# Kernel optimization log

Measured on AMD Instinct MI355X. Metric: run time of the kernel, lower is better.

## Reference

```python
import jax, jax.numpy as jnp
import numpy as np

B, T, C, H = 1, 1024, 2048, 32
N = C // H  # head_dim = 64
EPS_GN = 0.00064


def setup_inputs() -> dict:
    key = jax.random.key(0)
    ks = jax.random.split(key, 40)
    f32 = jnp.float32

    def rn(k, shape, s):
        return jax.random.normal(k, shape, f32) * s

    layer_idx, n_layer = 12, 24
    r01 = layer_idx / (n_layer - 1)
    r1a0 = 1.0 - layer_idx / n_layer
    ddd = (jnp.arange(C, dtype=f32) / C).reshape(1, 1, C)
    decay_speed = -7.0 + 5.0 * (jnp.arange(C, dtype=f32) / (C - 1)) ** (0.85 + r01 ** 0.5)

    inp = dict(
        hidden_states=jax.random.normal(ks[0], (B, T, C), f32),
        Wq=rn(ks[1], (C, C), 0.02), Wk=rn(ks[2], (C, C), 0.02),
        Wv=rn(ks[3], (C, C), 0.02), Wo=rn(ks[4], (C, C), 0.02),
        time_maa_x=1.0 - ddd ** (0.6 * r1a0 ** 0.9),
        time_maa_rg=rn(ks[5], (1, 1, C), 0.01),
        time_maa_wa=rn(ks[6], (1, 1, C), 0.01),
        time_maa_k=rn(ks[7], (1, 1, C), 0.01),
        time_maa_v=rn(ks[8], (1, 1, C), 0.01),
        time_maa_w1=rn(ks[9], (C, 4 * 32), 0.01),
        time_maa_w2=rn(ks[10], (4, 32, C), 0.01),
        time_decay=decay_speed.reshape(1, 1, C) + 0.5,
        time_decay_w1=rn(ks[11], (C, 64), 0.01),
        time_decay_w2=rn(ks[12], (64, C), 0.01),
        time_aaaaa=rn(ks[13], (1, 1, C), 0.01),
        time_aaa_w1=rn(ks[14], (C, 16), 0.01),
        time_aaa_w2=rn(ks[15], (16, C), 0.01),
        time_kkk_w1=rn(ks[16], (C, 16), 0.01),
        time_kkk_w2=rn(ks[17], (16, C), 0.01),
        gate_w1=rn(ks[18], (C, 128), 0.01),
        gate_w2=rn(ks[19], (128, C), 0.01),
        time_misc_a=rn(ks[20], (1, 1, C), 0.01),
        ma_w1=rn(ks[21], (C, 16), 0.01),
        ma_w2=rn(ks[22], (16, C), 0.01),
        time_misc_k=rn(ks[23], (1, 1, C), 0.01),
        mk_w1=rn(ks[24], (C, 16), 0.01),
        mk_w2=rn(ks[25], (16, C), 0.01),
        time_faaaa=rn(ks[26], (1, 1, H, N), 0.01),
        ln_w=1.0 + rn(ks[27], (C,), 0.01),
        ln_b=rn(ks[28], (C,), 0.01),
    )
    return inp


def _wkv7(r, w, k, v, a, b):
    """RWKV7 matrix-state recurrence. Inputs [B,T,C]; per head state [N,N].
    state_t = state * exp(w_t) (per key-col) + (state @ a_t) b_t^T + v_t k_t^T;
    out_t = state_t @ r_t."""
    hs = lambda x: x.reshape(B, T, H, N)
    r, k, v, a, b = map(hs, (r, k, v, a, b))
    dec = jnp.exp(hs(w))  # w <= -0.5, decay in (0,1)

    def step(state, inp):
        r_t, d_t, k_t, v_t, a_t, b_t = inp  # each [B,H,N]
        sa = jnp.einsum('bhij,bhj->bhi', state, a_t)
        state = (state * d_t[:, :, None, :]
                 + sa[..., None] * b_t[:, :, None, :]
                 + v_t[..., None] * k_t[:, :, None, :])
        out = jnp.einsum('bhij,bhj->bhi', state, r_t)
        return state, out

    xs = tuple(jnp.moveaxis(t, 1, 0) for t in (r, dec, k, v, a, b))  # [T,B,H,N]
    state0 = jnp.zeros((B, H, N, N), r.dtype)
    _, out = jax.lax.scan(step, state0, xs)
    return jnp.moveaxis(out, 0, 1).reshape(B, T, C)


def _group_norm(x, w, b):
    xg = x.reshape(B, T, H, N)
    mu = xg.mean(-1, keepdims=True)
    var = xg.var(-1, keepdims=True)
    xn = (xg - mu) * jax.lax.rsqrt(var + EPS_GN)
    return xn.reshape(B, T, C) * w + b


def reference(hidden_states, Wq, Wk, Wv, Wo, time_maa_x, time_maa_rg, time_maa_wa,
              time_maa_k, time_maa_v, time_maa_w1, time_maa_w2, time_decay,
              time_decay_w1, time_decay_w2, time_aaaaa, time_aaa_w1, time_aaa_w2,
              time_kkk_w1, time_kkk_w2, gate_w1, gate_w2, time_misc_a, ma_w1, ma_w2,
              time_misc_k, mk_w1, mk_w2, time_faaaa, ln_w, ln_b):
    x = hidden_states  # T already multiple of 16, so no padding branch
    dxprev = jnp.pad(x, ((0, 0), (1, 0), (0, 0)))[:, :-1] - x  # token shift
    xxx = x + dxprev * time_maa_x
    mix = jnp.tanh(xxx @ time_maa_w1).reshape(B, T, 4, 32)
    mix = jnp.einsum('btfd,fdc->fbtc', mix, time_maa_w2)  # [4,B,T,C]
    mrg, mwa, mk_mix, mv = mix[0], mix[1], mix[2], mix[3]
    xrg = x + dxprev * (time_maa_rg + mrg)
    xwa = x + dxprev * (time_maa_wa + mwa)
    xk = x + dxprev * (time_maa_k + mk_mix)
    xv = x + dxprev * (time_maa_v + mv)

    r = xrg @ Wq
    w = -jax.nn.softplus(-(time_decay + jnp.tanh(xwa @ time_decay_w1) @ time_decay_w2)) - 0.5
    k = xk @ Wk
    v = xv @ Wv
    g = jnp.tanh(xrg @ gate_w1) @ gate_w2

    kk = k + jnp.tanh(xk @ time_kkk_w1) @ time_kkk_w2
    kkh = kk.reshape(B, T, H, N)
    kk = (kkh / jnp.maximum(jnp.linalg.norm(kkh, axis=-1, keepdims=True), 1e-12)).reshape(B, T, C)

    a = jax.nn.sigmoid(time_aaaaa + (xwa @ time_aaa_w1) @ time_aaa_w2)
    ma = jax.nn.sigmoid(time_misc_a + (xwa @ ma_w1) @ ma_w2)
    k = k * ma + k * a * (1.0 - ma)
    mk_g = jax.nn.sigmoid(time_misc_k + (xk @ mk_w1) @ mk_w2)
    k = k * jnp.exp(jnp.minimum(w * mk_g, 0.0))

    y = _wkv7(r, w, k, v, -kk, kk * a)
    y = _group_norm(y, ln_w, ln_b)
    rh, kh, vh = (t.reshape(B, T, H, N) for t in (r, k, v))
    y = y + ((rh * kh * time_faaaa).sum(-1, keepdims=True) * vh).reshape(B, T, C)
    return (y * g) @ Wo
```

## Files before the change

### kernel.cpp

```cpp
#include <hip/hip_runtime.h>


#define T_ 1024
#define C_ 2048
#define H_ 32
#define N_ 64

using half8  = __attribute__((ext_vector_type(8))) _Float16;
using half4  = __attribute__((ext_vector_type(4))) _Float16;
using floatx4 = __attribute__((ext_vector_type(4))) float;

#define DPP_ADD(v, ctrl) \
    ((v) + __int_as_float(__builtin_amdgcn_update_dpp( \
        0, __float_as_int(v), (ctrl), 0xf, 0xf, true)))
#define REDUCE16(v) do { \
    v = DPP_ADD(v, 0xB1); v = DPP_ADD(v, 0x4E); \
    v = DPP_ADD(v, 0x141); v = DPP_ADD(v, 0x140); } while (0)

__device__ __forceinline__ void async_cp16(const void* g, void* l) {
    __builtin_amdgcn_global_load_lds(
        (const __attribute__((address_space(1))) void*)g,
        (__attribute__((address_space(3))) void*)l, 16, 0, 0);
}

__global__ __launch_bounds__(256) void k_tr(
    const float* __restrict__ W0, const float* __restrict__ W1,
    const float* __restrict__ W2, const float* __restrict__ W3,
    _Float16* __restrict__ D0, _Float16* __restrict__ D1,
    _Float16* __restrict__ D2, _Float16* __restrict__ D3)
{
    const int z = blockIdx.z;
    const float* S = (z == 0) ? W0 : (z == 1) ? W1 : (z == 2) ? W2 : W3;
    _Float16* D = (z == 0) ? D0 : (z == 1) ? D1 : (z == 2) ? D2 : D3;
    const int nb = blockIdx.x * 64, kb = blockIdx.y * 64;
    __shared__ __align__(16) float tile[64][65];
    const int tr = threadIdx.x >> 4, tc4 = (threadIdx.x & 15) * 4;
#pragma unroll
    for (int p = 0; p < 4; ++p) {
        int row = p * 16 + tr;
        float4 v = *(const float4*)&S[(size_t)(kb + row) * C_ + nb + tc4];
        tile[row][tc4 + 0] = v.x; tile[row][tc4 + 1] = v.y;
        tile[row][tc4 + 2] = v.z; tile[row][tc4 + 3] = v.w;
    }
    __syncthreads();
#pragma unroll
    for (int p = 0; p < 4; ++p) {
        int n = p * 16 + tr;
        half4 u;
        u[0] = (_Float16)tile[tc4 + 0][n];
        u[1] = (_Float16)tile[tc4 + 1][n];
        u[2] = (_Float16)tile[tc4 + 2][n];
        u[3] = (_Float16)tile[tc4 + 3][n];
        *(half4*)&D[(size_t)(nb + n) * C_ + kb + tc4] = u;
    }
}

__global__ __launch_bounds__(256) void k_trW(
    const float* __restrict__ maa_w1, const float* __restrict__ gate_w1,
    const float* __restrict__ decay_w1, const float* __restrict__ aaa_w1,
    const float* __restrict__ ma_w1, const float* __restrict__ kkk_w1,
    const float* __restrict__ mk_w1,
    _Float16* __restrict__ WTm, _Float16* __restrict__ WTl)
{
    const int z = blockIdx.z;
    const int k = blockIdx.x * 256 + threadIdx.x;
    const int n = blockIdx.y;
    if (z == 0 && n >= 128) return;
    const float* src; int stride, col;
    _Float16* dst;
    if (z == 0) { src = maa_w1; stride = 128; col = n; dst = WTm; }
    else {
        dst = WTl;
        if (n < 128)      { src = gate_w1;  stride = 128; col = n; }
        else if (n < 192) { src = decay_w1; stride = 64;  col = n - 128; }
        else if (n < 208) { src = aaa_w1;   stride = 16;  col = n - 192; }
        else if (n < 224) { src = ma_w1;    stride = 16;  col = n - 208; }
        else if (n < 240) { src = kkk_w1;   stride = 16;  col = n - 224; }
        else              { src = mk_w1;    stride = 16;  col = n - 240; }
    }
    dst[(size_t)n * C_ + k] = (_Float16)src[(size_t)k * stride + col];
}

__global__ __launch_bounds__(256) void k_prep(
    const float* __restrict__ X, const float* __restrict__ maa_x,
    _Float16* __restrict__ xxxH)
{
    const size_t idx = (size_t)blockIdx.x * 256 + threadIdx.x;
    const int c = (int)(idx & (C_ - 1));
    float cur = X[idx];
    float prev = (idx >= C_) ? X[idx - C_] : 0.0f;
    xxxH[idx] = (_Float16)(cur + (prev - cur) * maa_x[c]);
}

__global__ __launch_bounds__(256) void k_lora(
    int which,
    const _Float16* __restrict__ Axxx, const _Float16* __restrict__ Axrg,
    const _Float16* __restrict__ Axwa, const _Float16* __restrict__ Axk,
    const _Float16* __restrict__ WTm, const _Float16* __restrict__ WTl,
    float* __restrict__ m1p, float* __restrict__ l2p)
{
    const int mt = blockIdx.x;
    const int nt = blockIdx.y;
    const int ks = blockIdx.z;
    const _Float16* A; const _Float16* BT; float* O; int ostride;
    if (which == 0) { A = Axxx; BT = WTm; O = m1p; ostride = 128; }
    else {
        BT = WTl; O = l2p; ostride = 256;
        A = (nt < 4) ? Axrg : (nt < 7) ? Axwa : Axk;
    }
    O += (size_t)ks * T_ * ostride;
    const int m0 = mt * 64, n0 = nt * 32, k0 = ks * 512;
    const int tid = threadIdx.x;
    __shared__ __align__(16) _Float16 As[64 * 40];
    __shared__ __align__(16) _Float16 Bs[32 * 40];
    const int lane = tid & 63, wv = tid >> 6;
    const int r16 = lane & 15, q = lane >> 4;

    floatx4 acc[2];
    { floatx4 zv = {0.f, 0.f, 0.f, 0.f}; acc[0] = zv; acc[1] = zv; }

    const int arow = tid >> 2, ac8 = (tid & 3) * 8;
    const _Float16* ag = A + (size_t)(m0 + arow) * C_ + k0 + ac8;
    const _Float16* bg = BT + (size_t)(n0 + (tid >> 2)) * C_ + k0 + ac8;

    for (int kc = 0; kc < 512; kc += 32) {
        half8 av = *(const half8*)(ag + kc);
        half8 bv;
        if (tid < 128) bv = *(const half8*)(bg + kc);
        *(half8*)&As[arow * 40 + ac8] = av;
        if (tid < 128) *(half8*)&Bs[(tid >> 2) * 40 + ac8] = bv;
        __syncthreads();
        half8 af = *(const half8*)&As[(wv * 16 + r16) * 40 + q * 8];
        half8 b0 = *(const half8*)&Bs[(r16) * 40 + q * 8];
        half8 b1 = *(const half8*)&Bs[(16 + r16) * 40 + q * 8];
        acc[0] = __builtin_amdgcn_mfma_f32_16x16x32_f16(af, b0, acc[0], 0, 0, 0);
        acc[1] = __builtin_amdgcn_mfma_f32_16x16x32_f16(af, b1, acc[1], 0, 0, 0);
        __syncthreads();
    }
#pragma unroll
    for (int j = 0; j < 2; ++j)
#pragma unroll
        for (int e = 0; e < 4; ++e) {
            int row = m0 + wv * 16 + q * 4 + e;
            int col = n0 + j * 16 + r16;
            O[(size_t)row * ostride + col] = acc[j][e];
        }
}

__global__ __launch_bounds__(256) void k_xmix(
    const float* __restrict__ X, const float* __restrict__ m1p,
    const float* __restrict__ w2,
    const float* __restrict__ mrg, const float* __restrict__ mwa,
    const float* __restrict__ mk, const float* __restrict__ mv,
    _Float16* __restrict__ xrgH, _Float16* __restrict__ xwaH,
    _Float16* __restrict__ xkH, _Float16* __restrict__ xvH)
{
    const int tid = threadIdx.x;
    const int c = blockIdx.x * 256 + tid;
    const int t0 = blockIdx.y * 16;
    const size_t P = (size_t)T_ * 128;
    __shared__ __align__(16) float m1s[16][128];
#pragma unroll
    for (int p = 0; p < 2; ++p) {
        int id = tid + p * 256;
        int r = id >> 5, c4 = (id & 31) * 4;
        size_t off = (size_t)(t0 + r) * 128 + c4;
        float4 v0 = *(const float4*)&m1p[off];
        float4 v1 = *(const float4*)&m1p[P + off];
        float4 v2 = *(const float4*)&m1p[2 * P + off];
        float4 v3 = *(const float4*)&m1p[3 * P + off];
        float4 v;
        v.x = tanhf(((v0.x + v1.x) + v2.x) + v3.x);
        v.y = tanhf(((v0.y + v1.y) + v2.y) + v3.y);
        v.z = tanhf(((v0.z + v1.z) + v2.z) + v3.z);
        v.w = tanhf(((v0.w + v1.w) + v2.w) + v3.w);
        *(float4*)&m1s[r][c4] = v;
    }
    __syncthreads();
    float a0[16], a1[16], a2[16], a3[16];
#pragma unroll
    for (int t = 0; t < 16; ++t) { a0[t] = 0.f; a1[t] = 0.f; a2[t] = 0.f; a3[t] = 0.f; }
    for (int d = 0; d < 32; ++d) {
        float w0 = w2[(size_t)(0 * 32 + d) * C_ + c];
        float w1 = w2[(size_t)(1 * 32 + d) * C_ + c];
        float w2v = w2[(size_t)(2 * 32 + d) * C_ + c];
        float w3 = w2[(size_t)(3 * 32 + d) * C_ + c];
#pragma unroll
        for (int t = 0; t < 16; ++t) {
            a0[t] = fmaf(m1s[t][d],      w0,  a0[t]);
            a1[t] = fmaf(m1s[t][32 + d], w1,  a1[t]);
            a2[t] = fmaf(m1s[t][64 + d], w2v, a2[t]);
            a3[t] = fmaf(m1s[t][96 + d], w3,  a3[t]);
        }
    }
    float vrg = mrg[c], vwa = mwa[c], vmk = mk[c], vmv = mv[c];
    float prev = (t0 > 0) ? X[(size_t)(t0 - 1) * C_ + c] : 0.0f;
    for (int t = 0; t < 16; ++t) {
        size_t idx = (size_t)(t0 + t) * C_ + c;
        float cur = X[idx];
        float dx = prev - cur;
        xrgH[idx] = (_Float16)(cur + dx * (vrg + a0[t]));
        xwaH[idx] = (_Float16)(cur + dx * (vwa + a1[t]));
        xkH[idx]  = (_Float16)(cur + dx * (vmk + a2[t]));
        xvH[idx]  = (_Float16)(cur + dx * (vmv + a3[t]));
        prev = cur;
    }
}

__global__ __launch_bounds__(256) void k_gemm(
    const _Float16* __restrict__ A0, const _Float16* __restrict__ B0, float* __restrict__ C0,
    const _Float16* __restrict__ A1, const _Float16* __restrict__ B1, float* __restrict__ C1,
    const _Float16* __restrict__ A2, const _Float16* __restrict__ B2, float* __restrict__ C2)
{
    const int z = blockIdx.z;
    const _Float16* A = (z == 0) ? A0 : (z == 1) ? A1 : A2;
    const _Float16* Bt = (z == 0) ? B0 : (z == 1) ? B1 : B2;
    float* C = (z == 0) ? C0 : (z == 1) ? C1 : C2;
    const int mtile = blockIdx.y * 128;
    const int ntile = blockIdx.x * 64;
    const int tid = threadIdx.x;
    __shared__ __align__(16) _Float16 As[2][128 * 32];
    __shared__ __align__(16) _Float16 Bs[2][64 * 32];
    const int lane = tid & 63;
    const int wvid = tid >> 6;
    const int wm = wvid >> 1, wn = wvid & 1;
    const int r16 = lane & 15, q = lane >> 4;
    const int qs = (q ^ ((r16 >> 1) & 3)) * 8;

    floatx4 acc[4][2];
#pragma unroll
    for (int i = 0; i < 4; ++i)
#pragma unroll
        for (int j = 0; j < 2; ++j) { floatx4 zv = {0.f, 0.f, 0.f, 0.f}; acc[i][j] = zv; }

    const int srow = tid >> 2, sq = tid & 3;
    const int sqg = (sq ^ ((srow >> 1) & 3)) * 8;
    const _Float16* agA = A + (size_t)(mtile + srow) * C_ + sqg;
    const _Float16* agB = Bt + (size_t)(ntile + srow) * C_ + sqg;
    const int ldso = srow * 32 + sq * 8;
    const size_t rowoff = (size_t)64 * C_;

    async_cp16(agA, &As[0][ldso]);
    async_cp16(agA + rowoff, &As[0][ldso + 64 * 32]);
    async_cp16(agB, &Bs[0][ldso]);

    for (int kc = 0; kc < C_; kc += 32) {
        const int p = (kc >> 5) & 1;
        __syncthreads();
        if (kc + 32 < C_) {
            async_cp16(agA + kc + 32, &As[p ^ 1][ldso]);
            async_cp16(agA + kc + 32 + rowoff, &As[p ^ 1][ldso + 64 * 32]);
            async_cp16(agB + kc + 32, &Bs[p ^ 1][ldso]);
        }
        half8 af[4], bf[2];
#pragma unroll
        for (int i = 0; i < 4; ++i)
            af[i] = *(const half8*)&As[p][(wm * 64 + i * 16 + r16) * 32 + qs];
#pragma unroll
        for (int j = 0; j < 2; ++j)
            bf[j] = *(const half8*)&Bs[p][(wn * 32 + j * 16 + r16) * 32 + qs];
#pragma unroll
        for (int i = 0; i < 4; ++i)
#pragma unroll
            for (int j = 0; j < 2; ++j)
                acc[i][j] = __builtin_amdgcn_mfma_f32_16x16x32_f16(af[i], bf[j], acc[i][j], 0, 0, 0);
    }
#pragma unroll
    for (int i = 0; i < 4; ++i)
#pragma unroll
        for (int j = 0; j < 2; ++j)
#pragma unroll
            for (int e = 0; e < 4; ++e) {
                int row = mtile + wm * 64 + i * 16 + q * 4 + e;
                int col = ntile + wn * 32 + j * 16 + r16;
                C[(size_t)row * C_ + col] = acc[i][j][e];
            }
}

__global__ __launch_bounds__(256) void k_fuse(
    const float* __restrict__ l2p,
    float* __restrict__ K0,
    const float* __restrict__ decay_w2, const float* __restrict__ aaa_w2,
    const float* __restrict__ ma_w2, const float* __restrict__ kkk_w2,
    const float* __restrict__ mk_w2,
    const float* __restrict__ tdecay, const float* __restrict__ aaaaa,
    const float* __restrict__ misc_a, const float* __restrict__ misc_k,
    float* __restrict__ Dout, float* __restrict__ KKout, float* __restrict__ Bout)
{
    const int tid = threadIdx.x;
    const int c = blockIdx.x * 256 + tid;
    const int t0 = blockIdx.y * 4;
    const size_t P = (size_t)T_ * 256;
    __shared__ __align__(16) float wsS[4][96];
    __shared__ __align__(16) float ksS[4][32];
    if (tid < 4 * 24) {
        int r = tid / 24, c4 = (tid % 24) * 4;
        size_t off = (size_t)(t0 + r) * 256 + 128 + c4;
        float4 v0 = *(const float4*)&l2p[off];
        float4 v1 = *(const float4*)&l2p[P + off];
        float4 v2 = *(const float4*)&l2p[2 * P + off];
        float4 v3 = *(const float4*)&l2p[3 * P + off];
        float4 v;
        v.x = ((v0.x + v1.x) + v2.x) + v3.x;
        v.y = ((v0.y + v1.y) + v2.y) + v3.y;
        v.z = ((v0.z + v1.z) + v2.z) + v3.z;
        v.w = ((v0.w + v1.w) + v2.w) + v3.w;
        if (c4 < 64) { v.x = tanhf(v.x); v.y = tanhf(v.y); v.z = tanhf(v.z); v.w = tanhf(v.w); }
        *(float4*)&wsS[r][c4] = v;
    }
    if (tid < 4 * 8) {
        int r = tid / 8, c4 = (tid % 8) * 4;
        size_t off = (size_t)(t0 + r) * 256 + 224 + c4;
        float4 v0 = *(const float4*)&l2p[off];
        float4 v1 = *(const float4*)&l2p[P + off];
        float4 v2 = *(const float4*)&l2p[2 * P + off];
        float4 v3 = *(const float4*)&l2p[3 * P + off];
        float4 v;
        v.x = ((v0.x + v1.x) + v2.x) + v3.x;
        v.y = ((v0.y + v1.y) + v2.y) + v3.y;
        v.z = ((v0.z + v1.z) + v2.z) + v3.z;
        v.w = ((v0.w + v1.w) + v2.w) + v3.w;
        if (c4 < 16) { v.x = tanhf(v.x); v.y = tanhf(v.y); v.z = tanhf(v.z); v.w = tanhf(v.w); }
        *(float4*)&ksS[r][c4] = v;
    }
    __syncthreads();
    float accW[4], accA[4], accMA[4], accKK[4], accMK[4];
#pragma unroll
    for (int r = 0; r < 4; ++r) { accW[r] = 0.f; accA[r] = 0.f; accMA[r] = 0.f; accKK[r] = 0.f; accMK[r] = 0.f; }
    for (int j = 0; j < 64; ++j) {
        float w = decay_w2[(size_t)j * C_ + c];
#pragma unroll
        for (int r = 0; r < 4; ++r) accW[r] = fmaf(wsS[r][j], w, accW[r]);
    }
    for (int j = 0; j < 16; ++j) {
        float wa = aaa_w2[(size_t)j * C_ + c];
        float wm = ma_w2[(size_t)j * C_ + c];
        float wk = kkk_w2[(size_t)j * C_ + c];
        float wq = mk_w2[(size_t)j * C_ + c];
#pragma unroll
        for (int r = 0; r < 4; ++r) {
            accA[r]  = fmaf(wsS[r][64 + j], wa, accA[r]);
            accMA[r] = fmaf(wsS[r][80 + j], wm, accMA[r]);
            accKK[r] = fmaf(ksS[r][j],      wk, accKK[r]);
            accMK[r] = fmaf(ksS[r][16 + j], wq, accMK[r]);
        }
    }
    float td = tdecay[c], aa = aaaaa[c], mia = misc_a[c], mik = misc_k[c];
#pragma unroll
    for (int r = 0; r < 4; ++r) {
        size_t idx = (size_t)(t0 + r) * C_ + c;
        float wraw = td + accW[r];
        float w = -__logf(1.0f + __expf(-wraw)) - 0.5f;
        float a  = 1.0f / (1.0f + __expf(-(aa  + accA[r])));
        float mav = 1.0f / (1.0f + __expf(-(mia + accMA[r])));
        float mkv = 1.0f / (1.0f + __expf(-(mik + accMK[r])));
        float k0 = K0[idx];
        float kkun = k0 + accKK[r];
        float ss = kkun * kkun;
        REDUCE16(ss);
        ss += __shfl_xor(ss, 16, 64);
        ss += __shfl_xor(ss, 32, 64);
        float kn = kkun * (1.0f / fmaxf(sqrtf(ss), 1e-12f));
        Dout[idx]  = __expf(w);
        KKout[idx] = kn;
        Bout[idx]  = kn * a;
        K0[idx]    = k0 * (mav + a * (1.0f - mav)) * __expf(fminf(w * mkv, 0.0f));
    }
}

__global__ __launch_bounds__(512) void k_wkv_p1(
    const float* __restrict__ DEC, const float* __restrict__ K,
    const float* __restrict__ V, const float* __restrict__ KK,
    const float* __restrict__ Bb,
    float* __restrict__ Send, float* __restrict__ Pend)
{
    const int tid = threadIdx.x;
    const int g = blockIdx.x;
    const int h = blockIdx.y;
    const int c0 = h * 64;
    const int wv = tid >> 6, lane = tid & 63;
    const int jg = lane & 15, q = lane >> 4, j4 = jg * 4;
    const bool isS = wv < 4;
    const int row0 = (isS ? wv : wv - 4) * 16 + q * 4;

    __shared__ __align__(16) float dS[2][16][64], kS[2][16][64], vS[2][16][64],
                                   aS[2][16][64], bS[2][16][64];

    const int pos = tid & 255, grp = tid >> 8;
    const int pst = pos >> 4, pq4 = (pos & 15) * 4;

#define P1_STAGE(buf, tcb) do {                                               \
    size_t gg = (size_t)((tcb) + pst) * C_ + c0 + pq4;                        \
    if (grp == 0) { async_cp16(&DEC[gg], &dS[buf][pst][pq4]);                 \
                    async_cp16(&KK[gg],  &aS[buf][pst][pq4]);                 \
                    async_cp16(&Bb[gg],  &bS[buf][pst][pq4]); }               \
    else          { async_cp16(&K[gg], &kS[buf][pst][pq4]);                   \
                    async_cp16(&V[gg], &vS[buf][pst][pq4]); }                 \
} while (0)

    float4 s0, s1, s2, s3;
    if (isS) {
        s0 = make_float4(0.f, 0.f, 0.f, 0.f); s1 = s0; s2 = s0; s3 = s0;
    } else {
#define IDROW(m) make_float4((j4 + 0 == row0 + (m)) ? 1.f : 0.f,              \
                             (j4 + 1 == row0 + (m)) ? 1.f : 0.f,              \
                             (j4 + 2 == row0 + (m)) ? 1.f : 0.f,              \
                             (j4 + 3 == row0 + (m)) ? 1.f : 0.f)
        s0 = IDROW(0); s1 = IDROW(1); s2 = IDROW(2); s3 = IDROW(3);
#undef IDROW
    }

    const int t0 = g * 128;
    P1_STAGE(0, t0);

    for (int tc = 0; tc < 128; tc += 16) {
        const int p = (tc >> 4) & 1;
        __syncthreads();
        if (tc + 16 < 128) P1_STAGE(p ^ 1, t0 + tc + 16);
#pragma unroll
        for (int tt = 0; tt < 16; ++tt) {
            float4 cd = *(float4*)&dS[p][tt][j4];
            float4 ca = *(float4*)&aS[p][tt][j4];
            float4 cb = *(float4*)&bS[p][tt][j4];
            float4 ck, vv;
            if (isS) {
                ck = *(float4*)&kS[p][tt][j4];
                vv = *(float4*)&vS[p][tt][row0];
            } else {
                ck = make_float4(0.f, 0.f, 0.f, 0.f);
                vv = make_float4(0.f, 0.f, 0.f, 0.f);
            }
            float sa0 = -(fmaf(s0.y, ca.y, s0.x * ca.x) + fmaf(s0.w, ca.w, s0.z * ca.z));
            float sa1 = -(fmaf(s1.y, ca.y, s1.x * ca.x) + fmaf(s1.w, ca.w, s1.z * ca.z));
            float sa2 = -(fmaf(s2.y, ca.y, s2.x * ca.x) + fmaf(s2.w, ca.w, s2.z * ca.z));
            float sa3 = -(fmaf(s3.y, ca.y, s3.x * ca.x) + fmaf(s3.w, ca.w, s3.z * ca.z));
            REDUCE16(sa0); REDUCE16(sa1); REDUCE16(sa2); REDUCE16(sa3);
            s0.x = fmaf(s0.x, cd.x, fmaf(sa0, cb.x, vv.x * ck.x));
            s0.y = fmaf(s0.y, cd.y, fmaf(sa0, cb.y, vv.x * ck.y));
            s0.z = fmaf(s0.z, cd.z, fmaf(sa0, cb.z, vv.x * ck.z));
            s0.w = fmaf(s0.w, cd.w, fmaf(sa0, cb.w, vv.x * ck.w));
            s1.x = fmaf(s1.x, cd.x, fmaf(sa1, cb.x, vv.y * ck.x));
            s1.y = fmaf(s1.y, cd.y, fmaf(sa1, cb.y, vv.y * ck.y));
            s1.z = fmaf(s1.z, cd.z, fmaf(sa1, cb.z, vv.y * ck.z));
            s1.w = fmaf(s1.w, cd.w, fmaf(sa1, cb.w, vv.y * ck.w));
            s2.x = fmaf(s2.x, cd.x, fmaf(sa2, cb.x, vv.z * ck.x));
            s2.y = fmaf(s2.y, cd.y, fmaf(sa2, cb.y, vv.z * ck.y));
            s2.z = fmaf(s2.z, cd.z, fmaf(sa2, cb.z, vv.z * ck.z));
            s2.w = fmaf(s2.w, cd.w, fmaf(sa2, cb.w, vv.z * ck.w));
            s3.x = fmaf(s3.x, cd.x, fmaf(sa3, cb.x, vv.w * ck.x));
            s3.y = fmaf(s3.y, cd.y, fmaf(sa3, cb.y, vv.w * ck.y));
            s3.z = fmaf(s3.z, cd.z, fmaf(sa3, cb.z, vv.w * ck.z));
            s3.w = fmaf(s3.w, cd.w, fmaf(sa3, cb.w, vv.w * ck.w));
        }
    }
    float* dst = isS ? Send : Pend;
    size_t base = (size_t)((h * 7 + g) * 64 + row0) * 64 + j4;
    *(float4*)&dst[base +   0] = s0;
    *(float4*)&dst[base +  64] = s1;
    *(float4*)&dst[base + 128] = s2;
    *(float4*)&dst[base + 192] = s3;
#undef P1_STAGE
}

__global__ __launch_bounds__(256) void k_wkv_comb(
    const float* __restrict__ Send, const float* __restrict__ Pend,
    float* __restrict__ Sin)
{
    const int h = blockIdx.x;
    const int tid = threadIdx.x;
    const int i = tid >> 2;
    const int jq = (tid & 3) * 16;
    __shared__ float Sc[64][65];
    __shared__ __align__(16) float Pl[64][64];

    float4 z4 = make_float4(0.f, 0.f, 0.f, 0.f);
#pragma unroll
    for (int c = 0; c < 16; c += 4)
        *(float4*)&Sin[(size_t)(h * 8) * 4096 + (size_t)i * 64 + jq + c] = z4;
#pragma unroll
    for (int c = 0; c < 16; ++c) Sc[i][jq + c] = 0.f;
    __syncthreads();

    for (int g = 1; g < 8; ++g) {
        const float* Pg = &Pend[(size_t)(h * 7 + g - 1) * 4096];
        for (int idx = tid * 4; idx < 4096; idx += 1024) {
            float4 v = *(const float4*)&Pg[idx];
            *(float4*)&Pl[idx >> 6][idx & 63] = v;
        }
        __syncthreads();
        float acc[16];
        const float* Sg = &Send[(size_t)(h * 7 + g - 1) * 4096 + (size_t)i * 64 + jq];
#pragma unroll
        for (int c = 0; c < 16; c += 4) {
            float4 v = *(const float4*)&Sg[c];
            acc[c] = v.x; acc[c + 1] = v.y; acc[c + 2] = v.z; acc[c + 3] = v.w;
        }
        for (int k = 0; k < 64; ++k) {
            float sik = Sc[i][k];
#pragma unroll
            for (int c = 0; c < 16; ++c) acc[c] = fmaf(sik, Pl[k][jq + c], acc[c]);
        }
        __syncthreads();
        float* So = &Sin[(size_t)(h * 8 + g) * 4096 + (size_t)i * 64 + jq];
#pragma unroll
        for (int c = 0; c < 16; ++c) Sc[i][jq + c] = acc[c];
#pragma unroll
        for (int c = 0; c < 16; c += 4) {
            float4 v = make_float4(acc[c], acc[c + 1], acc[c + 2], acc[c + 3]);
            *(float4*)&So[c] = v;
        }
        __syncthreads();
    }
}

__global__ __launch_bounds__(256) void k_wkv_p2(
    const float* __restrict__ R, const float* __restrict__ DEC,
    const float* __restrict__ K, const float* __restrict__ V,
    const float* __restrict__ KK, const float* __restrict__ Bb,
    const float* __restrict__ Sin, float* __restrict__ Y)
{
    const int tid = threadIdx.x;
    const int g = blockIdx.x;
    const int h = blockIdx.y;
    const int c0 = h * 64;
    const int wv = tid >> 6, lane = tid & 63;
    const int jg = lane & 15, q = lane >> 4, j4 = jg * 4;
    const int row0 = wv * 16 + q * 4;

    __shared__ __align__(16) float rS[2][16][64], dS[2][16][64], kS[2][16][64],
                                   aS[2][16][64], bS[2][16][64], vS[2][16][64];

    const int pst = tid >> 4, pq4 = (tid & 15) * 4;

#define P2_STAGE(buf, tcb) do {                                               \
    size_t gg = (size_t)((tcb) + pst) * C_ + c0 + pq4;                        \
    async_cp16(&R[gg],   &rS[buf][pst][pq4]);                                 \
    async_cp16(&DEC[gg], &dS[buf][pst][pq4]);                                 \
    async_cp16(&K[gg],   &kS[buf][pst][pq4]);                                 \
    async_cp16(&V[gg],   &vS[buf][pst][pq4]);                                 \
    async_cp16(&KK[gg],  &aS[buf][pst][pq4]);                                 \
    async_cp16(&Bb[gg],  &bS[buf][pst][pq4]);                                 \
} while (0)

    float4 s0, s1, s2, s3;
    {
        const float* Sb = &Sin[(size_t)((h * 8 + g) * 64 + row0) * 64 + j4];
        s0 = *(const float4*)&Sb[0];
        s1 = *(const float4*)&Sb[64];
        s2 = *(const float4*)&Sb[128];
        s3 = *(const float4*)&Sb[192];
    }

    const int t0 = g * 128;
    P2_STAGE(0, t0);

    for (int tc = 0; tc < 128; tc += 16) {
        const int p = (tc >> 4) & 1;
        __syncthreads();
        if (tc + 16 < 128) P2_STAGE(p ^ 1, t0 + tc + 16);
#pragma unroll
        for (int hh = 0; hh < 2; ++hh) {
            float po0[8], po1[8], po2[8], po3[8];
#pragma unroll
            for (int qs2 = 0; qs2 < 8; ++qs2) {
                const int tt = hh * 8 + qs2;
                float4 cr = *(float4*)&rS[p][tt][j4];
                float4 cd = *(float4*)&dS[p][tt][j4];
                float4 ck = *(float4*)&kS[p][tt][j4];
                float4 ca = *(float4*)&aS[p][tt][j4];
                float4 cb = *(float4*)&bS[p][tt][j4];
                float4 vv = *(float4*)&vS[p][tt][row0];
                float sa0 = -(fmaf(s0.y, ca.y, s0.x * ca.x) + fmaf(s0.w, ca.w, s0.z * ca.z));
                float sa1 = -(fmaf(s1.y, ca.y, s1.x * ca.x) + fmaf(s1.w, ca.w, s1.z * ca.z));
                float sa2 = -(fmaf(s2.y, ca.y, s2.x * ca.x) + fmaf(s2.w, ca.w, s2.z * ca.z));
                float sa3 = -(fmaf(s3.y, ca.y, s3.x * ca.x) + fmaf(s3.w, ca.w, s3.z * ca.z));
                REDUCE16(sa0); REDUCE16(sa1); REDUCE16(sa2); REDUCE16(sa3);
                s0.x = fmaf(s0.x, cd.x, fmaf(sa0, cb.x, vv.x * ck.x));
                s0.y = fmaf(s0.y, cd.y, fmaf(sa0, cb.y, vv.x * ck.y));
                s0.z = fmaf(s0.z, cd.z, fmaf(sa0, cb.z, vv.x * ck.z));
                s0.w = fmaf(s0.w, cd.w, fmaf(sa0, cb.w, vv.x * ck.w));
                s1.x = fmaf(s1.x, cd.x, fmaf(sa1, cb.x, vv.y * ck.x));
                s1.y = fmaf(s1.y, cd.y, fmaf(sa1, cb.y, vv.y * ck.y));
                s1.z = fmaf(s1.z, cd.z, fmaf(sa1, cb.z, vv.y * ck.z));
                s1.w = fmaf(s1.w, cd.w, fmaf(sa1, cb.w, vv.y * ck.w));
                s2.x = fmaf(s2.x, cd.x, fmaf(sa2, cb.x, vv.z * ck.x));
                s2.y = fmaf(s2.y, cd.y, fmaf(sa2, cb.y, vv.z * ck.y));
                s2.z = fmaf(s2.z, cd.z, fmaf(sa2, cb.z, vv.z * ck.z));
                s2.w = fmaf(s2.w, cd.w, fmaf(sa2, cb.w, vv.z * ck.w));
                s3.x = fmaf(s3.x, cd.x, fmaf(sa3, cb.x, vv.w * ck.x));
                s3.y = fmaf(s3.y, cd.y, fmaf(sa3, cb.y, vv.w * ck.y));
                s3.z = fmaf(s3.z, cd.z, fmaf(sa3, cb.z, vv.w * ck.z));
                s3.w = fmaf(s3.w, cd.w, fmaf(sa3, cb.w, vv.w * ck.w));
                po0[qs2] = fmaf(s0.w, cr.w, fmaf(s0.z, cr.z, fmaf(s0.y, cr.y, s0.x * cr.x)));
                po1[qs2] = fmaf(s1.w, cr.w, fmaf(s1.z, cr.z, fmaf(s1.y, cr.y, s1.x * cr.x)));
                po2[qs2] = fmaf(s2.w, cr.w, fmaf(s2.z, cr.z, fmaf(s2.y, cr.y, s2.x * cr.x)));
                po3[qs2] = fmaf(s3.w, cr.w, fmaf(s3.z, cr.z, fmaf(s3.y, cr.y, s3.x * cr.x)));
            }
#pragma unroll
            for (int qs2 = 0; qs2 < 8; ++qs2) {
                REDUCE16(po0[qs2]); REDUCE16(po1[qs2]);
                REDUCE16(po2[qs2]); REDUCE16(po3[qs2]);
            }
            if (jg == 0) {
#pragma unroll
                for (int qs2 = 0; qs2 < 8; ++qs2) {
                    float4 o = make_float4(po0[qs2], po1[qs2], po2[qs2], po3[qs2]);
                    *(float4*)&Y[(size_t)(t0 + tc + hh * 8 + qs2) * C_ + c0 + row0] = o;
                }
            }
        }
    }
#undef P2_STAGE
}

__global__ __launch_bounds__(256) void k_gn(
    const float* __restrict__ Y, const float* __restrict__ R, const float* __restrict__ K,
    const float* __restrict__ V, const float* __restrict__ l2p,
    const float* __restrict__ gw2,
    const float* __restrict__ faaaa, const float* __restrict__ lnw,
    const float* __restrict__ lnb, _Float16* __restrict__ YG)
{
    const int tid = threadIdx.x;
    const int c = blockIdx.x * 256 + tid;
    const int t0 = blockIdx.y * 16;
    const size_t P = (size_t)T_ * 256;
    __shared__ __align__(16) float gs[16][128];
    for (int id = tid; id < 16 * 128; id += 256) {
        int r = id >> 7, cc = id & 127;
        size_t off = (size_t)(t0 + r) * 256 + cc;
        float v = ((l2p[off] + l2p[P + off]) + l2p[2 * P + off]) + l2p[3 * P + off];
        gs[r][cc] = tanhf(v);
    }
    __syncthreads();
    float gacc[16];
#pragma unroll
    for (int r = 0; r < 16; ++r) gacc[r] = 0.f;
    for (int j = 0; j < 128; ++j) {
        float w = gw2[(size_t)j * C_ + c];
#pragma unroll
        for (int r = 0; r < 16; ++r) gacc[r] = fmaf(gs[r][j], w, gacc[r]);
    }
    float fa = faaaa[c], lw = lnw[c], lb = lnb[c];
    for (int r = 0; r < 16; ++r) {
        const size_t idx = (size_t)(t0 + r) * C_ + c;
        float y = Y[idx];
        float s1 = y, s2 = y * y;
#pragma unroll
        for (int off = 1; off < 64; off <<= 1) {
            s1 += __shfl_xor(s1, off, 64);
            s2 += __shfl_xor(s2, off, 64);
        }
        float mu = s1 * (1.0f / 64.0f);
        float var = s2 * (1.0f / 64.0f) - mu * mu;
        float gn = (y - mu) * rsqrtf(var + 0.00064f) * lw + lb;
        float p = R[idx] * K[idx] * fa;
#pragma unroll
        for (int off = 1; off < 64; off <<= 1) p += __shfl_xor(p, off, 64);
        float y2 = gn + p * V[idx];
        YG[idx] = (_Float16)(y2 * gacc[r]);
    }
}

extern "C" void kernel_launch(void* const* d_in, const int* in_sizes, int n_in,
                              void* d_out, int out_size, void* d_ws, size_t ws_size,
                              hipStream_t stream)
{
    (void)in_sizes; (void)n_in; (void)out_size; (void)ws_size;
    const float* hidden   = (const float*)d_in[0];
    const float* Wq       = (const float*)d_in[1];
    const float* Wk       = (const float*)d_in[2];
    const float* Wv       = (const float*)d_in[3];
    const float* Wo       = (const float*)d_in[4];
    const float* maa_x    = (const float*)d_in[5];
    const float* maa_rg   = (const float*)d_in[6];
    const float* maa_wa   = (const float*)d_in[7];
    const float* maa_k    = (const float*)d_in[8];
    const float* maa_v    = (const float*)d_in[9];
    const float* maa_w1   = (const float*)d_in[10];
    const float* maa_w2   = (const float*)d_in[11];
    const float* tdecay   = (const float*)d_in[12];
    const float* decay_w1 = (const float*)d_in[13];
    const float* decay_w2 = (const float*)d_in[14];
    const float* aaaaa    = (const float*)d_in[15];
    const float* aaa_w1   = (const float*)d_in[16];
    const float* aaa_w2   = (const float*)d_in[17];
    const float* kkk_w1   = (const float*)d_in[18];
    const float* kkk_w2   = (const float*)d_in[19];
    const float* gate_w1  = (const float*)d_in[20];
    const float* gate_w2  = (const float*)d_in[21];
    const float* misc_a   = (const float*)d_in[22];
    const float* ma_w1    = (const float*)d_in[23];
    const float* ma_w2    = (const float*)d_in[24];
    const float* misc_k   = (const float*)d_in[25];
    const float* mk_w1    = (const float*)d_in[26];
    const float* mk_w2    = (const float*)d_in[27];
    const float* faaaa    = (const float*)d_in[28];
    const float* lnw      = (const float*)d_in[29];
    const float* lnb      = (const float*)d_in[30];

    float* ws = (float*)d_ws;
    const size_t TC = (size_t)T_ * C_;
    float* S0 = ws + 0 * TC;
    float* Send = ws + 1 * TC;
    float* Pend = Send + (size_t)32 * 7 * 64 * 64;
    float* S2 = ws + 2 * TC;
    float* S3 = ws + 3 * TC;
    float* S4 = ws + 4 * TC;
    float* S5 = ws + 5 * TC;
    float* S6 = ws + 6 * TC;
    float* S7 = ws + 7 * TC;
    float* m1p = ws + 8 * TC;
    float* l2p = m1p + (size_t)4 * T_ * 128;
    _Float16* WTq = (_Float16*)(l2p + (size_t)4 * T_ * 256);
    _Float16* WTk = WTq + (size_t)C_ * C_;
    _Float16* WTv = WTk + (size_t)C_ * C_;
    _Float16* WTo = WTv + (size_t)C_ * C_;
    _Float16* WTm = WTo + (size_t)C_ * C_;
    _Float16* WTl = WTm + (size_t)128 * C_;
    _Float16* xxxH = WTl + (size_t)256 * C_;
    _Float16* xrgH = xxxH + TC;
    _Float16* xwaH = xrgH + TC;
    _Float16* xkH  = xwaH + TC;
    _Float16* xvH  = xkH + TC;
    _Float16* ygH  = xxxH;
    float* Sin = (float*)xrgH;
    float* out = (float*)d_out;

    k_tr<<<dim3(32, 32, 4), 256, 0, stream>>>(Wq, Wk, Wv, Wo, WTq, WTk, WTv, WTo);
    k_trW<<<dim3(8, 256, 2), 256, 0, stream>>>(maa_w1, gate_w1, decay_w1,
        aaa_w1, ma_w1, kkk_w1, mk_w1, WTm, WTl);
    k_prep<<<dim3((int)(TC / 256)), 256, 0, stream>>>(hidden, maa_x, xxxH);
    k_lora<<<dim3(16, 4, 4), 256, 0, stream>>>(0, xxxH, xxxH, xxxH, xxxH,
        WTm, WTl, m1p, l2p);
    k_xmix<<<dim3(8, 64), 256, 0, stream>>>(hidden, m1p, maa_w2,
        maa_rg, maa_wa, maa_k, maa_v, xrgH, xwaH, xkH, xvH);
    k_lora<<<dim3(16, 8, 4), 256, 0, stream>>>(1, xxxH, xrgH, xwaH, xkH,
        WTm, WTl, m1p, l2p);
    k_gemm<<<dim3(32, 8, 3), 256, 0, stream>>>(
        xrgH, WTq, S4,  xkH, WTk, S6,  xvH, WTv, S7);
    k_fuse<<<dim3(8, 256), 256, 0, stream>>>(l2p, S6, decay_w2, aaa_w2, ma_w2,
        kkk_w2, mk_w2, tdecay, aaaaa, misc_a, misc_k, S5, S3, S2);
    k_wkv_p1<<<dim3(7, 32), 512, 0, stream>>>(S5, S6, S7, S3, S2, Send, Pend);
    k_wkv_comb<<<dim3(32), 256, 0, stream>>>(Send, Pend, Sin);
    k_wkv_p2<<<dim3(8, 32), 256, 0, stream>>>(S4, S5, S6, S7, S3, S2, Sin, S0);
    k_gn<<<dim3(8, 64), 256, 0, stream>>>(S0, S4, S6, S7, l2p, gate_w2,
        faaaa, lnw, lnb, ygH);
    k_gemm<<<dim3(32, 8, 1), 256, 0, stream>>>(
        ygH, WTo, out,  ygH, WTo, out,  ygH, WTo, out);
}
```

Before: 513.2 us.

## Triple-buffer GEMM LDS loads with explicit vmcnt waits and barriers

The fp16 MFMA GEMM moves from a double-buffered async global-to-LDS pipeline to a three-stage ring, issuing loads two K-steps ahead. Explicit s_waitcnt vmcnt counts and raw s_barrier calls replace __syncthreads, so only the oldest stage's loads must land before compute. The aim is to hide more global-memory latency behind MFMA work. The cost is 50% more LDS per block, which may lower occupancy, and the hand-written wait counts must match the three loads issued per stage.

```diff
diff --git a/kernel.cpp b/kernel.cpp
--- a/kernel.cpp
+++ b/kernel.cpp
@@ -219,8 +219,8 @@
     const int mtile = blockIdx.y * 128;
     const int ntile = blockIdx.x * 64;
     const int tid = threadIdx.x;
-    __shared__ __align__(16) _Float16 As[2][128 * 32];
-    __shared__ __align__(16) _Float16 Bs[2][64 * 32];
+    __shared__ __align__(16) _Float16 As[3][128 * 32];
+    __shared__ __align__(16) _Float16 Bs[3][64 * 32];
     const int lane = tid & 63;
     const int wvid = tid >> 6;
     const int wm = wvid >> 1, wn = wvid & 1;
@@ -240,18 +240,22 @@
     const int ldso = srow * 32 + sq * 8;
     const size_t rowoff = (size_t)64 * C_;
 
-    async_cp16(agA, &As[0][ldso]);
-    async_cp16(agA + rowoff, &As[0][ldso + 64 * 32]);
-    async_cp16(agB, &Bs[0][ldso]);
-
-    for (int kc = 0; kc < C_; kc += 32) {
-        const int p = (kc >> 5) & 1;
-        __syncthreads();
-        if (kc + 32 < C_) {
-            async_cp16(agA + kc + 32, &As[p ^ 1][ldso]);
-            async_cp16(agA + kc + 32 + rowoff, &As[p ^ 1][ldso + 64 * 32]);
-            async_cp16(agB + kc + 32, &Bs[p ^ 1][ldso]);
-        }
+#define G_STAGE(pb, koff) do {                                                \
+        async_cp16(agA + (koff), &As[pb][ldso]);                              \
+        async_cp16(agA + (koff) + rowoff, &As[pb][ldso + 64 * 32]);           \
+        async_cp16(agB + (koff), &Bs[pb][ldso]);                              \
+    } while (0)
+
+    G_STAGE(0, 0);
+    G_STAGE(1, 32);
+    __builtin_amdgcn_sched_barrier(0);
+    asm volatile("s_waitcnt vmcnt(3)" ::: "memory");
+    __builtin_amdgcn_s_barrier();
+    __builtin_amdgcn_sched_barrier(0);
+
+    for (int ks = 0; ks < 64; ++ks) {
+        const int p = ks % 3;
+        if (ks + 2 < 64) G_STAGE((ks + 2) % 3, (ks + 2) * 32);
         half8 af[4], bf[2];
 #pragma unroll
         for (int i = 0; i < 4; ++i)
@@ -264,6 +268,13 @@
 #pragma unroll
             for (int j = 0; j < 2; ++j)
                 acc[i][j] = __builtin_amdgcn_mfma_f32_16x16x32_f16(af[i], bf[j], acc[i][j], 0, 0, 0);
+        __builtin_amdgcn_sched_barrier(0);
+        if (ks + 2 < 64)
+            asm volatile("s_waitcnt vmcnt(3)" ::: "memory");
+        else
+            asm volatile("s_waitcnt vmcnt(0)" ::: "memory");
+        __builtin_amdgcn_s_barrier();
+        __builtin_amdgcn_sched_barrier(0);
     }
 #pragma unroll
     for (int i = 0; i < 4; ++i)
@@ -275,6 +286,7 @@
                 int col = ntile + wn * 32 + j * 16 + r16;
                 C[(size_t)row * C_ + col] = acc[i][j][e];
             }
+#undef G_STAGE
 }
 
 __global__ __launch_bounds__(256) void k_fuse(
```

Result: no change. 515.3 us (+0.4%).
